# Optimization experiments

Measured on AMD Instinct MI355X. Metric: run time of the kernel, lower is better.

## Reference

```python
import jax, jax.numpy as jnp
import numpy as np

E, H, M = 1024, 16, 256
B, S = 2, 2048
D = E // H
SCALE = D ** -0.5


def setup_inputs() -> dict:
    key = jax.random.key(0)
    ks = jax.random.split(key, 10)
    p = 0.02
    return {
        "x": jax.random.normal(ks[0], (B, S, E), jnp.float32),
        "Wq": jax.random.normal(ks[1], (E, E), jnp.float32) * p,
        "bq": jax.random.normal(ks[2], (E,), jnp.float32) * p,
        "Wk": jax.random.normal(ks[3], (E, E), jnp.float32) * p,
        "bk": jax.random.normal(ks[4], (E,), jnp.float32) * p,
        "Wv": jax.random.normal(ks[5], (E, E), jnp.float32) * p,
        "bv": jax.random.normal(ks[6], (E,), jnp.float32) * p,
        "Wo": jax.random.normal(ks[7], (E, E), jnp.float32) * p,
        "bo": jax.random.normal(ks[8], (E,), jnp.float32) * p,
        "memory_state": jax.random.normal(ks[9], (M, E), jnp.float32) * p,
    }


def reference(x, Wq, bq, Wk, bk, Wv, bv, Wo, bo, memory_state):
    b, s, e = x.shape
    # QKV projections (torch Linear: y = x W^T + b), split heads -> [b,h,s,d]
    q = (x @ Wq.T + bq).reshape(b, s, H, D).transpose(0, 2, 1, 3)
    k = (x @ Wk.T + bk).reshape(b, s, H, D).transpose(0, 2, 1, 3)
    v = (x @ Wv.T + bv).reshape(b, s, H, D).transpose(0, 2, 1, 3)
    # full self-attention (eval mode: dropout is identity)
    attn = jax.nn.softmax(jnp.einsum("bhqd,bhkd->bhqk", q, k) * SCALE, axis=-1)
    attn_out = jnp.einsum("bhqk,bhkd->bhqd", attn, v)
    attn_out = attn_out.transpose(0, 2, 1, 3).reshape(b, s, e)
    # memory-read cross-attention on raw x against compressed memory [M,E]
    mem_w = jax.nn.softmax(jnp.einsum("bse,me->bsm", x, memory_state) * SCALE, axis=-1)
    mem_out = jnp.einsum("bsm,me->bse", mem_w, memory_state)
    out = attn_out + 0.5 * mem_out
    return out @ Wo.T + bo
```

## Files before the change

kernel.cpp:

```cpp
#include <hip/hip_runtime.h>
#include <cstdint>
#include <cstddef>


typedef __bf16 bf16;
typedef bf16  bf16x8 __attribute__((ext_vector_type(8)));
typedef bf16  bf16x4 __attribute__((ext_vector_type(4)));
typedef float f32x4  __attribute__((ext_vector_type(4)));

#define B_DIM 2
#define S_DIM 2048
#define E_DIM 1024
#define H_DIM 16
#define D_DIM 64
#define M_DIM 256
#define NROW  (B_DIM * S_DIM)
#define C1 0.18033688011112042f

__device__ __forceinline__ void async_cp16(const bf16* g, bf16* l)
{
    __builtin_amdgcn_global_load_lds(
        (const __attribute__((address_space(1))) void*)g,
        (__attribute__((address_space(3))) void*)l, 16, 0, 0);
}

__global__ void __launch_bounds__(256)
conv_all(const float* __restrict__ x,  const float* __restrict__ Wq,
         const float* __restrict__ Wk, const float* __restrict__ Wv,
         const float* __restrict__ Wo, const float* __restrict__ mem,
         bf16* __restrict__ xb,  bf16* __restrict__ Wqb,
         bf16* __restrict__ Wkb, bf16* __restrict__ Wvb,
         bf16* __restrict__ Wob, bf16* __restrict__ memb,
         bf16* __restrict__ memt)
{
    int t = blockIdx.x * 256 + threadIdx.x;
    const float* src; bf16* dst; int off; bool is_mem = false;
    if      (t <  524288) { src = x;   dst = xb;   off = t; }
    else if (t <  655360) { src = Wq;  dst = Wqb;  off = t - 524288; }
    else if (t <  786432) { src = Wk;  dst = Wkb;  off = t - 655360; }
    else if (t <  917504) { src = Wv;  dst = Wvb;  off = t - 786432; }
    else if (t < 1048576) { src = Wo;  dst = Wob;  off = t - 917504; }
    else                  { src = mem; dst = memb; off = t - 1048576; is_mem = true; }
    const float4* p = (const float4*)src + (size_t)off * 2;
    float4 a = p[0], b = p[1];
    bf16x8 o;
    o[0] = (bf16)a.x; o[1] = (bf16)a.y; o[2] = (bf16)a.z; o[3] = (bf16)a.w;
    o[4] = (bf16)b.x; o[5] = (bf16)b.y; o[6] = (bf16)b.z; o[7] = (bf16)b.w;
    *(bf16x8*)(dst + (size_t)off * 8) = o;
    if (is_mem) {
        int r = off >> 7, c0 = (off & 127) * 8;
        float h[8] = {a.x, a.y, a.z, a.w, b.x, b.y, b.z, b.w};
#pragma unroll
        for (int j = 0; j < 8; ++j)
            memt[(size_t)(c0 + j) * M_DIM + r] = (bf16)(0.5f * h[j]);
    }
}

struct GemmAcc { f32x4 a[4][4]; };

__device__ __forceinline__ void
gemm_core(const bf16* __restrict__ A, const bf16* __restrict__ Bm,
          int K, int m0, int n0, bf16* As, bf16* Bs, GemmAcc& R)
{
    const int tid  = threadIdx.x;
    const int lane = tid & 63;
    const int wave = tid >> 6;
    const int quad = lane >> 4;
    const int l16  = lane & 15;
    const int wm   = (wave >> 1) * 64;
    const int wn   = (wave & 1) * 64;

#pragma unroll
    for (int i = 0; i < 4; ++i)
#pragma unroll
        for (int j = 0; j < 4; ++j)
            R.a[i][j] = f32x4{0.f, 0.f, 0.f, 0.f};

    int s_c0  = wave * 128 + lane;
    int s_r0  = s_c0 >> 2;
    int s_k0  = (s_c0 & 3) ^ ((s_r0 >> 1) & 3);
    int s_c1  = s_c0 + 64;
    int s_r1  = s_c1 >> 2;
    int s_k1  = (s_c1 & 3) ^ ((s_r1 >> 1) & 3);
    const bf16* gA0 = A  + (size_t)(m0 + s_r0) * K + s_k0 * 8;
    const bf16* gA1 = A  + (size_t)(m0 + s_r1) * K + s_k1 * 8;
    const bf16* gB0 = Bm + (size_t)(n0 + s_r0) * K + s_k0 * 8;
    const bf16* gB1 = Bm + (size_t)(n0 + s_r1) * K + s_k1 * 8;

#define STAGE(buf, k0)                                                     \
    do {                                                                   \
        async_cp16(gA0 + (k0), &As[(buf) * 4096 + wave * 1024]);           \
        async_cp16(gA1 + (k0), &As[(buf) * 4096 + wave * 1024 + 512]);     \
        async_cp16(gB0 + (k0), &Bs[(buf) * 4096 + wave * 1024]);           \
        async_cp16(gB1 + (k0), &Bs[(buf) * 4096 + wave * 1024 + 512]);     \
    } while (0)

    STAGE(0, 0);
    int buf = 0;
    for (int k0 = 0; k0 < K; k0 += 32) {
        __syncthreads();
        if (k0 + 32 < K) STAGE(buf ^ 1, k0 + 32);

        const bf16* Ab = As + buf * 4096;
        const bf16* Bb = Bs + buf * 4096;
        bf16x8 af[4], bfr[4];
#pragma unroll
        for (int mi = 0; mi < 4; ++mi) {
            int m    = wm + mi * 16 + l16;
            int slot = quad ^ ((m >> 1) & 3);
            af[mi]   = *(const bf16x8*)(&Ab[(m * 4 + slot) * 8]);
        }
#pragma unroll
        for (int ni = 0; ni < 4; ++ni) {
            int n    = wn + ni * 16 + l16;
            int slot = quad ^ ((n >> 1) & 3);
            bfr[ni]  = *(const bf16x8*)(&Bb[(n * 4 + slot) * 8]);
        }
#pragma unroll
        for (int mi = 0; mi < 4; ++mi)
#pragma unroll
            for (int ni = 0; ni < 4; ++ni)
                R.a[mi][ni] = __builtin_amdgcn_mfma_f32_16x16x32_bf16(
                    af[mi], bfr[ni], R.a[mi][ni], 0, 0, 0);
        buf ^= 1;
    }
#undef STAGE
}

__global__ void __launch_bounds__(256, 3)
gemm_qkvl(const bf16* __restrict__ A,
          const bf16* __restrict__ Wq, const bf16* __restrict__ Wk,
          const bf16* __restrict__ Wv, const bf16* __restrict__ memb,
          const float* __restrict__ bq, const float* __restrict__ bk,
          const float* __restrict__ bv,
          bf16* __restrict__ q, bf16* __restrict__ k,
          bf16* __restrict__ vt, bf16* __restrict__ lg)
{
    __shared__ __align__(16) bf16 As[2 * 4096];
    __shared__ __align__(16) bf16 Bs[2 * 4096];
    const int x    = blockIdx.x;
    const int widx = (x < 24) ? (x >> 3) : 3;
    const int n0   = (x < 24) ? (x & 7) * 128 : (x - 24) * 128;
    const int m0   = blockIdx.y * 128;
    const bf16*  Bm = (widx == 0) ? Wq : (widx == 1) ? Wk :
                      (widx == 2) ? Wv : memb;
    GemmAcc R;
    gemm_core(A, Bm, E_DIM, m0, n0, As, Bs, R);

    const int lane = threadIdx.x & 63, wave = threadIdx.x >> 6;
    const int quad = lane >> 4, l16 = lane & 15;
    const int wm = (wave >> 1) * 64, wn = (wave & 1) * 64;

    if (widx == 0 || widx == 1) {
        bf16* C = (widx == 0) ? q : k;
        const float* bi = (widx == 0) ? bq : bk;
        float scale = (widx == 0) ? C1 : 1.0f;
#pragma unroll
        for (int ni = 0; ni < 4; ++ni) {
            int col  = n0 + wn + ni * 16 + l16;
            float bb = bi[col];
#pragma unroll
            for (int mi = 0; mi < 4; ++mi)
#pragma unroll
                for (int r = 0; r < 4; ++r) {
                    int rowg = m0 + wm + mi * 16 + quad * 4 + r;
                    C[(size_t)rowg * E_DIM + col] =
                        (bf16)((R.a[mi][ni][r] + bb) * scale);
                }
        }
    } else if (widx == 2) {
#pragma unroll
        for (int ni = 0; ni < 4; ++ni) {
            int col = n0 + wn + ni * 16 + l16;
            float bb = bv[col];
#pragma unroll
            for (int mi = 0; mi < 4; ++mi) {
                int row0 = m0 + wm + mi * 16 + quad * 4;
                int bidx = row0 >> 11, s = row0 & 2047;
                bf16x4 pk;
#pragma unroll
                for (int r = 0; r < 4; ++r) pk[r] = (bf16)(R.a[mi][ni][r] + bb);
                *(bf16x4*)(&vt[((size_t)(bidx * H_DIM) * 64 + col) * S_DIM + s]) = pk;
            }
        }
    } else {
#pragma unroll
        for (int ni = 0; ni < 4; ++ni) {
            int col = n0 + wn + ni * 16 + l16;
#pragma unroll
            for (int mi = 0; mi < 4; ++mi)
#pragma unroll
                for (int r = 0; r < 4; ++r) {
                    int rowg = m0 + wm + mi * 16 + quad * 4 + r;
                    lg[(size_t)rowg * M_DIM + col] = (bf16)R.a[mi][ni][r];
                }
        }
    }
}

__global__ void __launch_bounds__(256, 2)
gemm_out64(const bf16* __restrict__ A, const bf16* __restrict__ Bm,
           const float* __restrict__ bias, float* __restrict__ C)
{
    __shared__ __align__(16) bf16 As[2 * 2048];
    __shared__ __align__(16) bf16 Bs[2 * 4096];
    const int tid  = threadIdx.x;
    const int lane = tid & 63;
    const int wave = tid >> 6;
    const int quad = lane >> 4;
    const int l16  = lane & 15;
    const int wm   = (wave >> 1) * 32;
    const int wn   = (wave & 1) * 64;
    const int m0   = blockIdx.y * 64;
    const int n0   = blockIdx.x * 128;
    const int K    = E_DIM;

    f32x4 acc[2][4];
#pragma unroll
    for (int i = 0; i < 2; ++i)
#pragma unroll
        for (int j = 0; j < 4; ++j) acc[i][j] = f32x4{0.f, 0.f, 0.f, 0.f};

    int a_s  = wave * 64 + lane;
    int a_r  = a_s >> 2;
    int a_k  = (a_s & 3) ^ ((a_r >> 1) & 3);
    int b_s0 = wave * 128 + lane;
    int b_r0 = b_s0 >> 2;
    int b_k0 = (b_s0 & 3) ^ ((b_r0 >> 1) & 3);
    int b_s1 = b_s0 + 64;
    int b_r1 = b_s1 >> 2;
    int b_k1 = (b_s1 & 3) ^ ((b_r1 >> 1) & 3);
    const bf16* gA  = A  + (size_t)(m0 + a_r) * K + a_k * 8;
    const bf16* gB0 = Bm + (size_t)(n0 + b_r0) * K + b_k0 * 8;
    const bf16* gB1 = Bm + (size_t)(n0 + b_r1) * K + b_k1 * 8;

#define STAGE64(buf, k0)                                                   \
    do {                                                                   \
        async_cp16(gA  + (k0), &As[(buf) * 2048 + wave * 512]);            \
        async_cp16(gB0 + (k0), &Bs[(buf) * 4096 + wave * 1024]);           \
        async_cp16(gB1 + (k0), &Bs[(buf) * 4096 + wave * 1024 + 512]);     \
    } while (0)

    STAGE64(0, 0);
    int buf = 0;
    for (int k0 = 0; k0 < K; k0 += 32) {
        __syncthreads();
        if (k0 + 32 < K) STAGE64(buf ^ 1, k0 + 32);
        const bf16* Ab = As + buf * 2048;
        const bf16* Bb = Bs + buf * 4096;
        bf16x8 af[2], bfr[4];
#pragma unroll
        for (int mi = 0; mi < 2; ++mi) {
            int m    = wm + mi * 16 + l16;
            int slot = quad ^ ((m >> 1) & 3);
            af[mi]   = *(const bf16x8*)(&Ab[(m * 4 + slot) * 8]);
        }
#pragma unroll
        for (int ni = 0; ni < 4; ++ni) {
            int n    = wn + ni * 16 + l16;
            int slot = quad ^ ((n >> 1) & 3);
            bfr[ni]  = *(const bf16x8*)(&Bb[(n * 4 + slot) * 8]);
        }
#pragma unroll
        for (int mi = 0; mi < 2; ++mi)
#pragma unroll
            for (int ni = 0; ni < 4; ++ni)
                acc[mi][ni] = __builtin_amdgcn_mfma_f32_16x16x32_bf16(
                    af[mi], bfr[ni], acc[mi][ni], 0, 0, 0);
        buf ^= 1;
    }
#undef STAGE64

#pragma unroll
    for (int ni = 0; ni < 4; ++ni) {
        int col  = n0 + wn + ni * 16 + l16;
        float bb = bias[col];
#pragma unroll
        for (int mi = 0; mi < 2; ++mi)
#pragma unroll
            for (int r = 0; r < 4; ++r) {
                int rowg = m0 + wm + mi * 16 + quad * 4 + r;
                C[(size_t)rowg * E_DIM + col] = acc[mi][ni][r] + bb;
            }
    }
}

__global__ void __launch_bounds__(128, 2)
flash_attn(const bf16* __restrict__ q, const bf16* __restrict__ k,
           const bf16* __restrict__ vt, const bf16* __restrict__ lg,
           const bf16* __restrict__ memt, bf16* __restrict__ outc)
{
    __shared__ __align__(16) bf16 Ks[2 * 4096];
    __shared__ __align__(16) bf16 Vs[2 * 4096];
    const int tid  = threadIdx.x;
    const int lane = tid & 63;
    const int wave = tid >> 6;
    const int quad = lane >> 4;
    const int l16  = lane & 15;
    const int lid = blockIdx.x;
    const int xcd = lid & 7;
    const int kk  = lid >> 3;
    const int qt  = kk & 31;
    const int p   = ((kk >> 5) << 3) | xcd;
    const int b   = p >> 4;
    const int h   = p & 15;
    const int q0  = qt * 64 + wave * 32;

    const bf16* qb = q  + (size_t)(b * S_DIM + q0) * E_DIM + h * D_DIM;
    const bf16* kb = k  + (size_t)(b * S_DIM) * E_DIM + h * D_DIM;
    const bf16* vb = vt + (size_t)(b * H_DIM + h) * D_DIM * S_DIM;

    const bf16* gK[4];
    const bf16* gV[4];
#pragma unroll
    for (int j = 0; j < 4; ++j) {
        int s  = (wave * 4 + j) * 64 + lane;
        int r  = s >> 3;
        int gc = (s & 7) ^ (r & 7);
        gK[j] = kb + (size_t)r * E_DIM + gc * 8;
        gV[j] = vb + (size_t)r * S_DIM + gc * 8;
    }

#define STAGE_KV(buf, kt)                                                      \
    do {                                                                       \
        _Pragma("unroll")                                                      \
        for (int j = 0; j < 4; ++j) {                                          \
            async_cp16(gK[j] + (size_t)(kt) * E_DIM,                           \
                       &Ks[(buf) * 4096 + (wave * 4 + j) * 512]);              \
            async_cp16(gV[j] + (kt),                                           \
                       &Vs[(buf) * 4096 + (wave * 4 + j) * 512]);              \
        }                                                                      \
    } while (0)

    bf16x8 a_q[2][2];
#pragma unroll
    for (int mf = 0; mf < 2; ++mf)
#pragma unroll
        for (int kc = 0; kc < 2; ++kc)
            a_q[mf][kc] = *(const bf16x8*)(
                qb + (size_t)(mf * 16 + l16) * E_DIM + kc * 32 + quad * 8);

    f32x4 o_acc[2][4];
#pragma unroll
    for (int mf = 0; mf < 2; ++mf)
#pragma unroll
        for (int i = 0; i < 4; ++i) o_acc[mf][i] = f32x4{0.f, 0.f, 0.f, 0.f};
    float l_part[2] = {0.f, 0.f};

    STAGE_KV(0, 0);
    int buf = 0;
    for (int kt = 0; kt < S_DIM; kt += 64) {
        __syncthreads();
        if (kt + 64 < S_DIM) STAGE_KV(buf ^ 1, kt + 64);
        const bf16* Kb = Ks + buf * 4096;
        const bf16* Vb = Vs + buf * 4096;

        f32x4 sc[2][4];
#pragma unroll
        for (int nb = 0; nb < 4; ++nb) {
            int row = nb * 16 + l16;
            int sl0 = quad ^ (row & 7);
            int sl1 = (4 + quad) ^ (row & 7);
            bf16x8 bk0 = *(const bf16x8*)(&Kb[row * 64 + sl0 * 8]);
            bf16x8 bk1 = *(const bf16x8*)(&Kb[row * 64 + sl1 * 8]);
#pragma unroll
            for (int mf = 0; mf < 2; ++mf) {
                f32x4 a = f32x4{0.f, 0.f, 0.f, 0.f};
                a = __builtin_amdgcn_mfma_f32_16x16x32_bf16(bk0, a_q[mf][0], a, 0, 0, 0);
                a = __builtin_amdgcn_mfma_f32_16x16x32_bf16(bk1, a_q[mf][1], a, 0, 0, 0);
                sc[mf][nb] = a;
            }
        }

        asm volatile("s_waitcnt lgkmcnt(0)\n\ts_barrier" ::: "memory");

        bf16* pw = Ks + buf * 4096 + wave * 2048;
#pragma unroll
        for (int mf = 0; mf < 2; ++mf)
#pragma unroll
            for (int nb = 0; nb < 4; ++nb) {
                bf16x4 pk;
#pragma unroll
                for (int r = 0; r < 4; ++r) {
                    float e = exp2f(sc[mf][nb][r]);
                    l_part[mf] += e;
                    pk[r] = (bf16)e;
                }
                int slot = (nb * 2 + (quad >> 1)) ^ (l16 & 7);
                *(bf16x4*)(&pw[(mf * 16 + l16) * 64 + slot * 8 + (quad & 1) * 4]) = pk;
            }

        bf16x8 a_p[2][2];
#pragma unroll
        for (int mf = 0; mf < 2; ++mf)
#pragma unroll
            for (int kc = 0; kc < 2; ++kc) {
                int slot = (kc * 4 + quad) ^ (l16 & 7);
                a_p[mf][kc] = *(const bf16x8*)(&pw[(mf * 16 + l16) * 64 + slot * 8]);
            }

#pragma unroll
        for (int nd = 0; nd < 4; ++nd) {
            int row  = nd * 16 + l16;
            int sl0  = quad ^ (row & 7);
            int sl1  = (4 + quad) ^ (row & 7);
            bf16x8 bv0 = *(const bf16x8*)(&Vb[row * 64 + sl0 * 8]);
            bf16x8 bv1 = *(const bf16x8*)(&Vb[row * 64 + sl1 * 8]);
#pragma unroll
            for (int mf = 0; mf < 2; ++mf) {
                o_acc[mf][nd] = __builtin_amdgcn_mfma_f32_16x16x32_bf16(
                    a_p[mf][0], bv0, o_acc[mf][nd], 0, 0, 0);
                o_acc[mf][nd] = __builtin_amdgcn_mfma_f32_16x16x32_bf16(
                    a_p[mf][1], bv1, o_acc[mf][nd], 0, 0, 0);
            }
        }
        buf ^= 1;
    }
#undef STAGE_KV

    float linv[2][4];
#pragma unroll
    for (int mf = 0; mf < 2; ++mf) {
        float L = l_part[mf];
        L += __shfl_xor(L, 16);
        L += __shfl_xor(L, 32);
        float Li = 1.f / L;
#pragma unroll
        for (int r = 0; r < 4; ++r)
            linv[mf][r] = __shfl(Li, quad * 4 + r);
    }

    const bf16* Pr = lg   + (size_t)(b * S_DIM + q0) * M_DIM;
    const bf16* Mt = memt + (size_t)(h * D_DIM) * M_DIM;
    float msum[2] = {0.f, 0.f};
    bf16x8 ep[2][8];
#pragma unroll
    for (int kc = 0; kc < 8; ++kc)
#pragma unroll
        for (int mf = 0; mf < 2; ++mf) {
            bf16x8 raw = *(const bf16x8*)(
                Pr + (size_t)(mf * 16 + l16) * M_DIM + kc * 32 + quad * 8);
#pragma unroll
            for (int j = 0; j < 8; ++j) {
                float e = exp2f(C1 * (float)raw[j]);
                msum[mf] += e;
                ep[mf][kc][j] = (bf16)e;
            }
        }
    float minv[2][4];
#pragma unroll
    for (int mf = 0; mf < 2; ++mf) {
        float L = msum[mf];
        L += __shfl_xor(L, 16);
        L += __shfl_xor(L, 32);
        float Li = 1.f / L;
#pragma unroll
        for (int r = 0; r < 4; ++r)
            minv[mf][r] = __shfl(Li, quad * 4 + r);
    }
    f32x4 macc[2][4];
#pragma unroll
    for (int mf = 0; mf < 2; ++mf)
#pragma unroll
        for (int i = 0; i < 4; ++i) macc[mf][i] = f32x4{0.f, 0.f, 0.f, 0.f};
#pragma unroll
    for (int kc = 0; kc < 8; ++kc)
#pragma unroll
        for (int nd = 0; nd < 4; ++nd) {
            bf16x8 bm = *(const bf16x8*)(
                Mt + (size_t)(nd * 16 + l16) * M_DIM + kc * 32 + quad * 8);
#pragma unroll
            for (int mf = 0; mf < 2; ++mf)
                macc[mf][nd] = __builtin_amdgcn_mfma_f32_16x16x32_bf16(
                    ep[mf][kc], bm, macc[mf][nd], 0, 0, 0);
        }

    bf16* ob = outc + (size_t)(b * S_DIM + q0) * E_DIM + h * D_DIM;
#pragma unroll
    for (int mf = 0; mf < 2; ++mf)
#pragma unroll
        for (int nd = 0; nd < 4; ++nd)
#pragma unroll
            for (int r = 0; r < 4; ++r) {
                size_t off = (size_t)(mf * 16 + quad * 4 + r) * E_DIM + nd * 16 + l16;
                ob[off] = (bf16)(o_acc[mf][nd][r] * linv[mf][r] +
                                 macc[mf][nd][r] * minv[mf][r]);
            }
}

extern "C" void kernel_launch(void* const* d_in, const int* in_sizes, int n_in,
                              void* d_out, int out_size, void* d_ws, size_t ws_size,
                              hipStream_t stream)
{
    (void)in_sizes; (void)n_in; (void)out_size; (void)ws_size;
    const float* x   = (const float*)d_in[0];
    const float* Wq  = (const float*)d_in[1];
    const float* bq  = (const float*)d_in[2];
    const float* Wk  = (const float*)d_in[3];
    const float* bk  = (const float*)d_in[4];
    const float* Wv  = (const float*)d_in[5];
    const float* bv  = (const float*)d_in[6];
    const float* Wo  = (const float*)d_in[7];
    const float* bo  = (const float*)d_in[8];
    const float* mem = (const float*)d_in[9];
    float* out = (float*)d_out;

    bf16* w = (bf16*)d_ws;
    const size_t NE = (size_t)NROW * E_DIM;
    const size_t EE = (size_t)E_DIM * E_DIM;
    bf16* xb      = w;
    bf16* q_ws    = w + NE;
    bf16* k_ws    = w + 2 * NE;
    bf16* Wqb     = w + 3 * NE;
    bf16* Wkb     = Wqb + EE;
    bf16* Wkb2    = Wkb;
    bf16* Wvb     = Wkb + EE;
    bf16* Wob     = Wvb + EE;
    bf16* memb    = Wob + EE;
    bf16* lg_ws   = memb + (size_t)M_DIM * E_DIM;
    bf16* memt_ws = lg_ws + (size_t)NROW * M_DIM;
    (void)Wkb2;
    bf16* vt_ws = (bf16*)d_out;

    dim3 blk(256);

    conv_all<<<dim3(4224), blk, 0, stream>>>(
        x, Wq, Wk, Wv, Wo, mem, xb, Wqb, Wkb, Wvb, Wob, memb, memt_ws);

    gemm_qkvl<<<dim3(26, NROW / 128), blk, 0, stream>>>(
        xb, Wqb, Wkb, Wvb, memb, bq, bk, bv, q_ws, k_ws, vt_ws, lg_ws);

    flash_attn<<<dim3(1024), dim3(128), 0, stream>>>(
        q_ws, k_ws, vt_ws, lg_ws, memt_ws, q_ws);

    gemm_out64<<<dim3(E_DIM / 128, NROW / 64), blk, 0, stream>>>(
        q_ws, Wob, bo, out);
}
```

Measured before the change: 242.7 us.

## Split attention block into four 16-row waves and compute row sums via MFMA

The flash attention block now runs four waves of 16 query rows instead of two waves of 32, sharing the same 64-row K/V tile and cutting per-wave register state so more waves can be resident. The softmax row sums are computed by an extra MFMA against a vector of ones rather than scalar adds and cross-lane shuffles, for both self-attention and the memory read. V fragments are loaded before the barrier, and the P scratch is spread across both the K and V LDS buffers. This adds extra MFMA work and doubles the K/V LDS reads per query row, in exchange for higher occupancy and less VALU work.

```diff
diff --git a/kernel.cpp b/kernel.cpp
--- a/kernel.cpp
+++ b/kernel.cpp
@@ -285,7 +285,7 @@
     }
 }
 
-__global__ void __launch_bounds__(128, 2)
+__global__ void __launch_bounds__(256, 4)
 flash_attn(const bf16* __restrict__ q, const bf16* __restrict__ k,
            const bf16* __restrict__ vt, const bf16* __restrict__ lg,
            const bf16* __restrict__ memt, bf16* __restrict__ outc)
@@ -304,48 +304,44 @@
     const int p   = ((kk >> 5) << 3) | xcd;
     const int b   = p >> 4;
     const int h   = p & 15;
-    const int q0  = qt * 64 + wave * 32;
+    const int q0  = qt * 64 + wave * 16;
 
     const bf16* qb = q  + (size_t)(b * S_DIM + q0) * E_DIM + h * D_DIM;
     const bf16* kb = k  + (size_t)(b * S_DIM) * E_DIM + h * D_DIM;
     const bf16* vb = vt + (size_t)(b * H_DIM + h) * D_DIM * S_DIM;
 
-    const bf16* gK[4];
-    const bf16* gV[4];
-#pragma unroll
-    for (int j = 0; j < 4; ++j) {
-        int s  = (wave * 4 + j) * 64 + lane;
-        int r  = s >> 3;
-        int gc = (s & 7) ^ (r & 7);
-        gK[j] = kb + (size_t)r * E_DIM + gc * 8;
-        gV[j] = vb + (size_t)r * S_DIM + gc * 8;
-    }
-
-#define STAGE_KV(buf, kt)                                                      \
-    do {                                                                       \
-        _Pragma("unroll")                                                      \
-        for (int j = 0; j < 4; ++j) {                                          \
-            async_cp16(gK[j] + (size_t)(kt) * E_DIM,                           \
-                       &Ks[(buf) * 4096 + (wave * 4 + j) * 512]);              \
-            async_cp16(gV[j] + (kt),                                           \
-                       &Vs[(buf) * 4096 + (wave * 4 + j) * 512]);              \
-        }                                                                      \
+    const int s_s0 = wave * 128 + lane;
+    const int s_r0 = s_s0 >> 3;
+    const int s_g0 = (s_s0 & 7) ^ (s_r0 & 7);
+    const int s_s1 = s_s0 + 64;
+    const int s_r1 = s_s1 >> 3;
+    const int s_g1 = (s_s1 & 7) ^ (s_r1 & 7);
+    const bf16* gK0 = kb + (size_t)s_r0 * E_DIM + s_g0 * 8;
+    const bf16* gK1 = kb + (size_t)s_r1 * E_DIM + s_g1 * 8;
+    const bf16* gV0 = vb + (size_t)s_r0 * S_DIM + s_g0 * 8;
+    const bf16* gV1 = vb + (size_t)s_r1 * S_DIM + s_g1 * 8;
+
+#define STAGE_KV(buf, kt)                                                   \
+    do {                                                                    \
+        async_cp16(gK0 + (size_t)(kt) * E_DIM, &Ks[(buf) * 4096 + wave * 1024]);       \
+        async_cp16(gK1 + (size_t)(kt) * E_DIM, &Ks[(buf) * 4096 + wave * 1024 + 512]); \
+        async_cp16(gV0 + (kt), &Vs[(buf) * 4096 + wave * 1024]);            \
+        async_cp16(gV1 + (kt), &Vs[(buf) * 4096 + wave * 1024 + 512]);      \
     } while (0)
 
-    bf16x8 a_q[2][2];
-#pragma unroll
-    for (int mf = 0; mf < 2; ++mf)
-#pragma unroll
-        for (int kc = 0; kc < 2; ++kc)
-            a_q[mf][kc] = *(const bf16x8*)(
-                qb + (size_t)(mf * 16 + l16) * E_DIM + kc * 32 + quad * 8);
-
-    f32x4 o_acc[2][4];
-#pragma unroll
-    for (int mf = 0; mf < 2; ++mf)
-#pragma unroll
-        for (int i = 0; i < 4; ++i) o_acc[mf][i] = f32x4{0.f, 0.f, 0.f, 0.f};
-    float l_part[2] = {0.f, 0.f};
+    bf16x8 a_q[2];
+#pragma unroll
+    for (int kc = 0; kc < 2; ++kc)
+        a_q[kc] = *(const bf16x8*)(qb + (size_t)l16 * E_DIM + kc * 32 + quad * 8);
+
+    bf16x8 vones;
+#pragma unroll
+    for (int j = 0; j < 8; ++j) vones[j] = (bf16)1.0f;
+
+    f32x4 o_acc[4], osum;
+#pragma unroll
+    for (int i = 0; i < 4; ++i) o_acc[i] = f32x4{0.f, 0.f, 0.f, 0.f};
+    osum = f32x4{0.f, 0.f, 0.f, 0.f};
 
     STAGE_KV(0, 0);
     int buf = 0;
@@ -355,7 +351,7 @@
         const bf16* Kb = Ks + buf * 4096;
         const bf16* Vb = Vs + buf * 4096;
 
-        f32x4 sc[2][4];
+        f32x4 sc[4];
 #pragma unroll
         for (int nb = 0; nb < 4; ++nb) {
             int row = nb * 16 + l16;
@@ -363,129 +359,88 @@
             int sl1 = (4 + quad) ^ (row & 7);
             bf16x8 bk0 = *(const bf16x8*)(&Kb[row * 64 + sl0 * 8]);
             bf16x8 bk1 = *(const bf16x8*)(&Kb[row * 64 + sl1 * 8]);
-#pragma unroll
-            for (int mf = 0; mf < 2; ++mf) {
-                f32x4 a = f32x4{0.f, 0.f, 0.f, 0.f};
-                a = __builtin_amdgcn_mfma_f32_16x16x32_bf16(bk0, a_q[mf][0], a, 0, 0, 0);
-                a = __builtin_amdgcn_mfma_f32_16x16x32_bf16(bk1, a_q[mf][1], a, 0, 0, 0);
-                sc[mf][nb] = a;
+            f32x4 a = f32x4{0.f, 0.f, 0.f, 0.f};
+            a = __builtin_amdgcn_mfma_f32_16x16x32_bf16(bk0, a_q[0], a, 0, 0, 0);
+            a = __builtin_amdgcn_mfma_f32_16x16x32_bf16(bk1, a_q[1], a, 0, 0, 0);
+            sc[nb] = a;
+        }
+
+        bf16x8 bv[4][2];
+#pragma unroll
+        for (int nd = 0; nd < 4; ++nd)
+#pragma unroll
+            for (int kc = 0; kc < 2; ++kc) {
+                int row  = nd * 16 + l16;
+                int slot = (kc * 4 + quad) ^ (row & 7);
+                bv[nd][kc] = *(const bf16x8*)(&Vb[row * 64 + slot * 8]);
             }
-        }
 
         asm volatile("s_waitcnt lgkmcnt(0)\n\ts_barrier" ::: "memory");
 
-        bf16* pw = Ks + buf * 4096 + wave * 2048;
-#pragma unroll
-        for (int mf = 0; mf < 2; ++mf)
-#pragma unroll
-            for (int nb = 0; nb < 4; ++nb) {
-                bf16x4 pk;
-#pragma unroll
-                for (int r = 0; r < 4; ++r) {
-                    float e = exp2f(sc[mf][nb][r]);
-                    l_part[mf] += e;
-                    pk[r] = (bf16)e;
-                }
-                int slot = (nb * 2 + (quad >> 1)) ^ (l16 & 7);
-                *(bf16x4*)(&pw[(mf * 16 + l16) * 64 + slot * 8 + (quad & 1) * 4]) = pk;
-            }
-
-        bf16x8 a_p[2][2];
-#pragma unroll
-        for (int mf = 0; mf < 2; ++mf)
-#pragma unroll
-            for (int kc = 0; kc < 2; ++kc) {
-                int slot = (kc * 4 + quad) ^ (l16 & 7);
-                a_p[mf][kc] = *(const bf16x8*)(&pw[(mf * 16 + l16) * 64 + slot * 8]);
-            }
+        bf16* pw = ((wave < 2) ? Ks : Vs) + buf * 4096 + (wave & 1) * 2048;
+#pragma unroll
+        for (int nb = 0; nb < 4; ++nb) {
+            bf16x4 pk;
+#pragma unroll
+            for (int r = 0; r < 4; ++r) pk[r] = (bf16)exp2f(sc[nb][r]);
+            int slot = (nb * 2 + (quad >> 1)) ^ (l16 & 7);
+            *(bf16x4*)(&pw[l16 * 64 + slot * 8 + (quad & 1) * 4]) = pk;
+        }
+
+        bf16x8 a_p[2];
+#pragma unroll
+        for (int kc = 0; kc < 2; ++kc) {
+            int slot = (kc * 4 + quad) ^ (l16 & 7);
+            a_p[kc]  = *(const bf16x8*)(&pw[l16 * 64 + slot * 8]);
+        }
 
 #pragma unroll
         for (int nd = 0; nd < 4; ++nd) {
-            int row  = nd * 16 + l16;
-            int sl0  = quad ^ (row & 7);
-            int sl1  = (4 + quad) ^ (row & 7);
-            bf16x8 bv0 = *(const bf16x8*)(&Vb[row * 64 + sl0 * 8]);
-            bf16x8 bv1 = *(const bf16x8*)(&Vb[row * 64 + sl1 * 8]);
-#pragma unroll
-            for (int mf = 0; mf < 2; ++mf) {
-                o_acc[mf][nd] = __builtin_amdgcn_mfma_f32_16x16x32_bf16(
-                    a_p[mf][0], bv0, o_acc[mf][nd], 0, 0, 0);
-                o_acc[mf][nd] = __builtin_amdgcn_mfma_f32_16x16x32_bf16(
-                    a_p[mf][1], bv1, o_acc[mf][nd], 0, 0, 0);
-            }
-        }
+            o_acc[nd] = __builtin_amdgcn_mfma_f32_16x16x32_bf16(
+                a_p[0], bv[nd][0], o_acc[nd], 0, 0, 0);
+            o_acc[nd] = __builtin_amdgcn_mfma_f32_16x16x32_bf16(
+                a_p[1], bv[nd][1], o_acc[nd], 0, 0, 0);
+        }
+        osum = __builtin_amdgcn_mfma_f32_16x16x32_bf16(a_p[0], vones, osum, 0, 0, 0);
+        osum = __builtin_amdgcn_mfma_f32_16x16x32_bf16(a_p[1], vones, osum, 0, 0, 0);
         buf ^= 1;
     }
 #undef STAGE_KV
 
-    float linv[2][4];
-#pragma unroll
-    for (int mf = 0; mf < 2; ++mf) {
-        float L = l_part[mf];
-        L += __shfl_xor(L, 16);
-        L += __shfl_xor(L, 32);
-        float Li = 1.f / L;
-#pragma unroll
-        for (int r = 0; r < 4; ++r)
-            linv[mf][r] = __shfl(Li, quad * 4 + r);
-    }
+    float linv[4];
+#pragma unroll
+    for (int r = 0; r < 4; ++r) linv[r] = 1.f / osum[r];
 
     const bf16* Pr = lg   + (size_t)(b * S_DIM + q0) * M_DIM;
     const bf16* Mt = memt + (size_t)(h * D_DIM) * M_DIM;
-    float msum[2] = {0.f, 0.f};
-    bf16x8 ep[2][8];
-#pragma unroll
-    for (int kc = 0; kc < 8; ++kc)
-#pragma unroll
-        for (int mf = 0; mf < 2; ++mf) {
-            bf16x8 raw = *(const bf16x8*)(
-                Pr + (size_t)(mf * 16 + l16) * M_DIM + kc * 32 + quad * 8);
-#pragma unroll
-            for (int j = 0; j < 8; ++j) {
-                float e = exp2f(C1 * (float)raw[j]);
-                msum[mf] += e;
-                ep[mf][kc][j] = (bf16)e;
-            }
-        }
-    float minv[2][4];
-#pragma unroll
-    for (int mf = 0; mf < 2; ++mf) {
-        float L = msum[mf];
-        L += __shfl_xor(L, 16);
-        L += __shfl_xor(L, 32);
-        float Li = 1.f / L;
-#pragma unroll
-        for (int r = 0; r < 4; ++r)
-            minv[mf][r] = __shfl(Li, quad * 4 + r);
-    }
-    f32x4 macc[2][4];
-#pragma unroll
-    for (int mf = 0; mf < 2; ++mf)
-#pragma unroll
-        for (int i = 0; i < 4; ++i) macc[mf][i] = f32x4{0.f, 0.f, 0.f, 0.f};
-#pragma unroll
-    for (int kc = 0; kc < 8; ++kc)
+    f32x4 macc[4], msum;
+#pragma unroll
+    for (int i = 0; i < 4; ++i) macc[i] = f32x4{0.f, 0.f, 0.f, 0.f};
+    msum = f32x4{0.f, 0.f, 0.f, 0.f};
+#pragma unroll
+    for (int kc = 0; kc < 8; ++kc) {
+        bf16x8 raw = *(const bf16x8*)(Pr + (size_t)l16 * M_DIM + kc * 32 + quad * 8);
+        bf16x8 ep;
+#pragma unroll
+        for (int j = 0; j < 8; ++j) ep[j] = (bf16)exp2f(C1 * (float)raw[j]);
 #pragma unroll
         for (int nd = 0; nd < 4; ++nd) {
             bf16x8 bm = *(const bf16x8*)(
                 Mt + (size_t)(nd * 16 + l16) * M_DIM + kc * 32 + quad * 8);
-#pragma unroll
-            for (int mf = 0; mf < 2; ++mf)
-                macc[mf][nd] = __builtin_amdgcn_mfma_f32_16x16x32_bf16(
-                    ep[mf][kc], bm, macc[mf][nd], 0, 0, 0);
-        }
+            macc[nd] = __builtin_amdgcn_mfma_f32_16x16x32_bf16(
+                ep, bm, macc[nd], 0, 0, 0);
+        }
+        msum = __builtin_amdgcn_mfma_f32_16x16x32_bf16(ep, vones, msum, 0, 0, 0);
+    }
 
     bf16* ob = outc + (size_t)(b * S_DIM + q0) * E_DIM + h * D_DIM;
 #pragma unroll
-    for (int mf = 0; mf < 2; ++mf)
-#pragma unroll
-        for (int nd = 0; nd < 4; ++nd)
-#pragma unroll
-            for (int r = 0; r < 4; ++r) {
-                size_t off = (size_t)(mf * 16 + quad * 4 + r) * E_DIM + nd * 16 + l16;
-                ob[off] = (bf16)(o_acc[mf][nd][r] * linv[mf][r] +
-                                 macc[mf][nd][r] * minv[mf][r]);
-            }
+    for (int nd = 0; nd < 4; ++nd)
+#pragma unroll
+        for (int r = 0; r < 4; ++r) {
+            size_t off = (size_t)(quad * 4 + r) * E_DIM + nd * 16 + l16;
+            ob[off] = (bf16)(o_acc[nd][r] * linv[r] + macc[nd][r] / msum[r]);
+        }
 }
 
 extern "C" void kernel_launch(void* const* d_in, const int* in_sizes, int n_in,
@@ -513,13 +468,11 @@
     bf16* k_ws    = w + 2 * NE;
     bf16* Wqb     = w + 3 * NE;
     bf16* Wkb     = Wqb + EE;
-    bf16* Wkb2    = Wkb;
     bf16* Wvb     = Wkb + EE;
     bf16* Wob     = Wvb + EE;
     bf16* memb    = Wob + EE;
     bf16* lg_ws   = memb + (size_t)M_DIM * E_DIM;
     bf16* memt_ws = lg_ws + (size_t)NROW * M_DIM;
-    (void)Wkb2;
     bf16* vt_ws = (bf16*)d_out;
 
     dim3 blk(256);
@@ -530,7 +483,7 @@
     gemm_qkvl<<<dim3(26, NROW / 128), blk, 0, stream>>>(
         xb, Wqb, Wkb, Wvb, memb, bq, bk, bv, q_ws, k_ws, vt_ws, lg_ws);
 
-    flash_attn<<<dim3(1024), dim3(128), 0, stream>>>(
+    flash_attn<<<dim3(1024), blk, 0, stream>>>(
         q_ws, k_ws, vt_ws, lg_ws, memt_ws, q_ws);
 
     gemm_out64<<<dim3(E_DIM / 128, NROW / 64), blk, 0, stream>>>(
```

After: 232.2 us. -4.3%, faster.
